# Kernel optimization log

Measured on AMD Instinct MI355X. Metric: run time of the kernel, lower is better.

The kernel has to match this reference:

```python
import jax, jax.numpy as jnp
import numpy as np

BS, DX, DY = 64, 512, 512


def setup_inputs() -> dict:
    key = jax.random.key(0)
    k1, k2, k3, k4, k5 = jax.random.split(key, 5)
    # ~1/3 of bins are zero -> ragged nonzero counts per sample
    hist = jax.random.randint(k1, (BS, DX, DY), 0, 3).astype(jnp.float32)
    xlo = jax.random.uniform(k2, (BS,)) * -5.0
    ylo = jax.random.uniform(k3, (BS,)) * -5.0
    x_lims = jnp.stack([xlo, xlo + 1.0 + 9.0 * jax.random.uniform(k4, (BS,))], axis=1)
    y_lims = jnp.stack([ylo, ylo + 1.0 + 9.0 * jax.random.uniform(k5, (BS,))], axis=1)
    return {"hist": hist, "x_lims": x_lims, "y_lims": y_lims}


def _grids(hist, x_lims, y_lims):
    bs, dx, dy = hist.shape
    cxw = (x_lims[:, 1] - x_lims[:, 0]) / dx  # [bs]
    cyw = (y_lims[:, 1] - y_lims[:, 0]) / dy
    cx = (jnp.linspace(0.0, 1.0, dx)[None, :] * cxw[:, None] * (dx - 1)
          + x_lims[:, 0:1] + cxw[:, None] / 2.0)  # [bs, dx]
    cy = (jnp.linspace(0.0, 1.0, dy)[None, :] * cyw[:, None] * (dy - 1)
          + y_lims[:, 0:1] + cyw[:, None] / 2.0)  # [bs, dy]
    hc = jnp.clip(hist, 0.0, 1.0)
    grid_x = cx[:, :, None] * hc  # [bs, dx, dy]
    grid_y = cy[:, None, :] * hc
    return grid_x, grid_y


def reference(hist, x_lims, y_lims):
    # as_sequence=True path. Data-dependent pad_sequence length is not
    # jit-able, so we pad to the full grid length L=dx*dy; the first lens[b]
    # entries per row match torch's ragged output, the rest are zeros
    # (torch's pad value). Stream compaction = stable argsort on the mask.
    bs, dx, dy = hist.shape
    L = dx * dy
    grid_x, grid_y = _grids(hist, x_lims, y_lims)
    mask = (hist != 0).reshape(bs, L)
    order = jnp.argsort(jnp.where(mask, 0, 1).astype(jnp.int32), axis=1, stable=True)
    pc_x = jnp.take_along_axis(grid_x.reshape(bs, L), order, axis=1)
    pc_y = jnp.take_along_axis(grid_y.reshape(bs, L), order, axis=1)
    pc_w = jnp.take_along_axis(hist.reshape(bs, L), order, axis=1)
    pc_w = jnp.where(jnp.take_along_axis(mask, order, axis=1), pc_w, 0.0)
    pc_lens = mask.sum(axis=1).astype(jnp.int32)  # [bs]
    return jnp.stack([pc_x, pc_y], axis=-1), pc_w, pc_lens
```

## Files before the change

### kernel.cpp

```cpp
#include <hip/hip_runtime.h>

#define BS 64
#define DX 512
#define DY 512
#define L (DX * DY)
#define TILE 4096
#define T_PER_S (L / TILE)
#define THREADS 256
#define EPT (TILE / THREADS)

__global__ __launch_bounds__(THREADS) void htpc_count(
    const float* __restrict__ hist, int* __restrict__ tile_count) {
  const int tile = blockIdx.x;
  const size_t base = (size_t)tile * TILE + (size_t)threadIdx.x * EPT;
  const float4* h4 = (const float4*)(hist + base);

  int cnt = 0;
#pragma unroll
  for (int i = 0; i < EPT / 4; ++i) {
    float4 v = h4[i];
    cnt += (v.x != 0.f) + (v.y != 0.f) + (v.z != 0.f) + (v.w != 0.f);
  }
  const int lane = threadIdx.x & 63;
  const int wv = threadIdx.x >> 6;
#pragma unroll
  for (int d = 32; d > 0; d >>= 1) cnt += __shfl_down(cnt, d);
  __shared__ int ws[THREADS / 64];
  if (lane == 0) ws[wv] = cnt;
  __syncthreads();
  if (threadIdx.x == 0) {
    int s = 0;
#pragma unroll
    for (int i = 0; i < THREADS / 64; ++i) s += ws[i];
    tile_count[tile] = s;
  }
}

__global__ __launch_bounds__(64) void htpc_scan(
    const int* __restrict__ tile_count, int* __restrict__ tile_off,
    float* __restrict__ out_lens, int* __restrict__ lens_i) {
  const int b = blockIdx.x;
  const int t = threadIdx.x;
  const int c = tile_count[b * T_PER_S + t];
  int incl = c;
#pragma unroll
  for (int d = 1; d < 64; d <<= 1) {
    int n = __shfl_up(incl, d);
    if (t >= d) incl += n;
  }
  tile_off[b * T_PER_S + t] = incl - c;
  if (t == 63) {
    out_lens[b] = (float)incl;
    lens_i[b] = incl;
  }
}

__global__ __launch_bounds__(THREADS) void htpc_compact(
    const float* __restrict__ hist, const float* __restrict__ x_lims,
    const float* __restrict__ y_lims, const int* __restrict__ tile_off,
    float* __restrict__ out_pc, float* __restrict__ out_w) {
  __shared__ float2 spc[TILE];
  __shared__ float sw[TILE];
  __shared__ int wsum[THREADS / 64];

  const int tile = blockIdx.x;
  const int b = tile / T_PER_S;
  const size_t gbase = (size_t)tile * TILE + (size_t)threadIdx.x * EPT;
  const float4* h4 = (const float4*)(hist + gbase);

  float v[EPT];
#pragma unroll
  for (int i = 0; i < EPT / 4; ++i) {
    float4 a = h4[i];
    v[i * 4 + 0] = a.x;
    v[i * 4 + 1] = a.y;
    v[i * 4 + 2] = a.z;
    v[i * 4 + 3] = a.w;
  }
  int cnt = 0;
#pragma unroll
  for (int i = 0; i < EPT; ++i) cnt += (v[i] != 0.f);

  const int lane = threadIdx.x & 63;
  const int wv = threadIdx.x >> 6;
  int incl = cnt;
#pragma unroll
  for (int d = 1; d < 64; d <<= 1) {
    int n = __shfl_up(incl, d);
    if (lane >= d) incl += n;
  }
  if (lane == 63) wsum[wv] = incl;
  __syncthreads();
  int wbase = 0, total = 0;
#pragma unroll
  for (int i = 0; i < THREADS / 64; ++i) {
    int s = wsum[i];
    if (i < wv) wbase += s;
    total += s;
  }
  int r = wbase + (incl - cnt);

  const float xlo = x_lims[b * 2], xhi = x_lims[b * 2 + 1];
  const float ylo = y_lims[b * 2], yhi = y_lims[b * 2 + 1];
  const float cxw = (xhi - xlo) / DX;
  const float cyw = (yhi - ylo) / DY;

  const int lidx0 = (int)(gbase - (size_t)b * L);

#pragma unroll
  for (int i = 0; i < EPT; ++i) {
    if (v[i] != 0.f) {
      const int idx = lidx0 + i;
      const int ix = idx >> 9;
      const int iy = idx & 511;
      spc[r] = make_float2(xlo + cxw * ((float)ix + 0.5f),
                           ylo + cyw * ((float)iy + 0.5f));
      sw[r] = v[i];
      ++r;
    }
  }
  __syncthreads();

  const int off = tile_off[tile];
  float2* pc2 = (float2*)out_pc + (size_t)b * L;
  float* w = out_w + (size_t)b * L;
  for (int k = threadIdx.x; k < total; k += THREADS) {
    pc2[off + k] = spc[k];
    w[off + k] = sw[k];
  }
}

__global__ __launch_bounds__(THREADS) void htpc_tail(
    const int* __restrict__ lens_i, float* __restrict__ out_pc,
    float* __restrict__ out_w) {
  const int tile = blockIdx.x;
  const int b = tile / T_PER_S;
  const int t = tile % T_PER_S;
  const int len = lens_i[b];
  const int begin = t * TILE;
  if (begin + TILE <= len) return;

  float2* pc2 = (float2*)out_pc + (size_t)b * L;
  float* w = out_w + (size_t)b * L;
  for (int i = begin + threadIdx.x; i < begin + TILE; i += THREADS) {
    if (i >= len) {
      pc2[i] = make_float2(0.f, 0.f);
      w[i] = 0.f;
    }
  }
}

extern "C" void kernel_launch(void* const* d_in, const int* in_sizes, int n_in,
                              void* d_out, int out_size, void* d_ws,
                              size_t ws_size, hipStream_t stream) {
  const float* hist = (const float*)d_in[0];
  const float* x_lims = (const float*)d_in[1];
  const float* y_lims = (const float*)d_in[2];

  float* out = (float*)d_out;
  float* out_pc = out;
  float* out_w = out + (size_t)BS * L * 2;
  float* out_lens = out_w + (size_t)BS * L;

  int* tile_count = (int*)d_ws;
  int* tile_off = tile_count + BS * T_PER_S;
  int* lens_i = tile_off + BS * T_PER_S;

  htpc_count<<<BS * T_PER_S, THREADS, 0, stream>>>(hist, tile_count);
  htpc_scan<<<BS, 64, 0, stream>>>(tile_count, tile_off, out_lens, lens_i);
  htpc_compact<<<BS * T_PER_S, THREADS, 0, stream>>>(hist, x_lims, y_lims,
                                                     tile_off, out_pc, out_w);
  htpc_tail<<<BS * T_PER_S, THREADS, 0, stream>>>(lens_i, out_pc, out_w);
}
```

Before: 259.2 us.

## Fuse tail zero-fill into compaction and defer coordinate math to store loop

Merges the tail zero-padding kernel into the compaction kernel, so one launch goes away and lens/tile metadata is not reread in a separate pass. Shared memory now holds compact int indices instead of float2 coordinates, and the coordinates are computed during the coalesced write-out. Outputs are written with nontemporal stores. The count kernel switches to a strided, coalesced float4 access pattern. Each compaction block now also does zero-fill work, which adds per-block work in exchange for the saved launch and pass.

Result: slower. 264.7 us (+2.1%).

```diff
diff --git a/kernel.cpp b/kernel.cpp
--- a/kernel.cpp
+++ b/kernel.cpp
@@ -9,16 +9,17 @@
 #define THREADS 256
 #define EPT (TILE / THREADS)
 
+typedef float vfloat2 __attribute__((ext_vector_type(2)));
+
 __global__ __launch_bounds__(THREADS) void htpc_count(
     const float* __restrict__ hist, int* __restrict__ tile_count) {
   const int tile = blockIdx.x;
-  const size_t base = (size_t)tile * TILE + (size_t)threadIdx.x * EPT;
-  const float4* h4 = (const float4*)(hist + base);
+  const float4* h4 = (const float4*)(hist + (size_t)tile * TILE);
 
   int cnt = 0;
 #pragma unroll
-  for (int i = 0; i < EPT / 4; ++i) {
-    float4 v = h4[i];
+  for (int r = 0; r < EPT / 4; ++r) {
+    float4 v = h4[r * THREADS + threadIdx.x];
     cnt += (v.x != 0.f) + (v.y != 0.f) + (v.z != 0.f) + (v.w != 0.f);
   }
   const int lane = threadIdx.x & 63;
@@ -55,16 +56,18 @@
   }
 }
 
-__global__ __launch_bounds__(THREADS) void htpc_compact(
+__global__ __launch_bounds__(THREADS) void htpc_compact_tail(
     const float* __restrict__ hist, const float* __restrict__ x_lims,
     const float* __restrict__ y_lims, const int* __restrict__ tile_off,
-    float* __restrict__ out_pc, float* __restrict__ out_w) {
-  __shared__ float2 spc[TILE];
+    const int* __restrict__ lens_i, float* __restrict__ out_pc,
+    float* __restrict__ out_w) {
+  __shared__ int sidx[TILE];
   __shared__ float sw[TILE];
   __shared__ int wsum[THREADS / 64];
 
   const int tile = blockIdx.x;
   const int b = tile / T_PER_S;
+  const int t = tile % T_PER_S;
   const size_t gbase = (size_t)tile * TILE + (size_t)threadIdx.x * EPT;
   const float4* h4 = (const float4*)(hist + gbase);
 
@@ -100,53 +103,45 @@
   }
   int r = wbase + (incl - cnt);
 
-  const float xlo = x_lims[b * 2], xhi = x_lims[b * 2 + 1];
-  const float ylo = y_lims[b * 2], yhi = y_lims[b * 2 + 1];
-  const float cxw = (xhi - xlo) / DX;
-  const float cyw = (yhi - ylo) / DY;
-
   const int lidx0 = (int)(gbase - (size_t)b * L);
-
 #pragma unroll
   for (int i = 0; i < EPT; ++i) {
     if (v[i] != 0.f) {
-      const int idx = lidx0 + i;
-      const int ix = idx >> 9;
-      const int iy = idx & 511;
-      spc[r] = make_float2(xlo + cxw * ((float)ix + 0.5f),
-                           ylo + cyw * ((float)iy + 0.5f));
+      sidx[r] = lidx0 + i;
       sw[r] = v[i];
       ++r;
     }
   }
   __syncthreads();
 
+  const float xlo = x_lims[b * 2], xhi = x_lims[b * 2 + 1];
+  const float ylo = y_lims[b * 2], yhi = y_lims[b * 2 + 1];
+  const float cxw = (xhi - xlo) / DX;
+  const float cyw = (yhi - ylo) / DY;
+
   const int off = tile_off[tile];
-  float2* pc2 = (float2*)out_pc + (size_t)b * L;
+  vfloat2* pc2 = (vfloat2*)out_pc + (size_t)b * L;
   float* w = out_w + (size_t)b * L;
+
   for (int k = threadIdx.x; k < total; k += THREADS) {
-    pc2[off + k] = spc[k];
-    w[off + k] = sw[k];
+    const int idx = sidx[k];
+    const int ix = idx >> 9;
+    const int iy = idx & 511;
+    vfloat2 p;
+    p.x = xlo + cxw * ((float)ix + 0.5f);
+    p.y = ylo + cyw * ((float)iy + 0.5f);
+    __builtin_nontemporal_store(p, pc2 + (off + k));
+    __builtin_nontemporal_store(sw[k], w + (off + k));
   }
-}
 
-__global__ __launch_bounds__(THREADS) void htpc_tail(
-    const int* __restrict__ lens_i, float* __restrict__ out_pc,
-    float* __restrict__ out_w) {
-  const int tile = blockIdx.x;
-  const int b = tile / T_PER_S;
-  const int t = tile % T_PER_S;
   const int len = lens_i[b];
   const int begin = t * TILE;
-  if (begin + TILE <= len) return;
-
-  float2* pc2 = (float2*)out_pc + (size_t)b * L;
-  float* w = out_w + (size_t)b * L;
-  for (int i = begin + threadIdx.x; i < begin + TILE; i += THREADS) {
-    if (i >= len) {
-      pc2[i] = make_float2(0.f, 0.f);
-      w[i] = 0.f;
-    }
+  const int end = begin + TILE;
+  const int s0 = (len > begin) ? len : begin;
+  const vfloat2 z = {0.f, 0.f};
+  for (int i = s0 + (int)threadIdx.x; i < end; i += THREADS) {
+    __builtin_nontemporal_store(z, pc2 + i);
+    __builtin_nontemporal_store(0.f, w + i);
   }
 }
 
@@ -168,7 +163,6 @@
 
   htpc_count<<<BS * T_PER_S, THREADS, 0, stream>>>(hist, tile_count);
   htpc_scan<<<BS, 64, 0, stream>>>(tile_count, tile_off, out_lens, lens_i);
-  htpc_compact<<<BS * T_PER_S, THREADS, 0, stream>>>(hist, x_lims, y_lims,
-                                                     tile_off, out_pc, out_w);
-  htpc_tail<<<BS * T_PER_S, THREADS, 0, stream>>>(lens_i, out_pc, out_w);
+  htpc_compact_tail<<<BS * T_PER_S, THREADS, 0, stream>>>(
+      hist, x_lims, y_lims, tile_off, lens_i, out_pc, out_w);
 }
```
